# Performance work log

Measured on AMD Instinct MI355X. Metric: run time of the kernel, lower is better.

The kernel has to match this reference:

```python
import jax, jax.numpy as jnp
import numpy as np

B, S, D, H = 4, 2048, 1024, 16
DH = D // H
THETA = 10000.0
STD = (2.0 / (D + D)) ** 0.5


def _rope(x):
    # x: [..., S, DH]; positions are arange(S). Rotate interleaved pairs.
    half = DH // 2
    inv_freq = THETA ** (-jnp.arange(half, dtype=jnp.float32) * 2.0 / DH)  # [half]
    ang = jnp.arange(S, dtype=jnp.float32)[:, None] * inv_freq[None, :]   # [S, half]
    cos, sin = jnp.cos(ang), jnp.sin(ang)
    x1, x2 = x[..., 0::2], x[..., 1::2]
    o1 = x1 * cos - x2 * sin
    o2 = x1 * sin + x2 * cos
    return jnp.stack([o1, o2], axis=-1).reshape(x.shape)


def setup_inputs() -> dict:
    key = jax.random.key(0)
    kx, kq, kk, kv, ko = jax.random.split(key, 5)
    return {
        "x": jax.random.normal(kx, (B, S, D), dtype=jnp.float32),
        "wq": jax.random.normal(kq, (D, D), dtype=jnp.float32) * STD,
        "wk": jax.random.normal(kk, (D, D), dtype=jnp.float32) * STD,
        "wv": jax.random.normal(kv, (D, D), dtype=jnp.float32) * STD,
        "wo": jax.random.normal(ko, (D, D), dtype=jnp.float32) * STD,
    }


def reference(x, wq, wk, wv, wo):
    # fused QKV projection (Linear with no bias: x @ W.T)
    wqkv = jnp.concatenate([wq, wk, wv], axis=0)          # [3D, D]
    qkv = jnp.einsum('bsd,ed->bse', x, wqkv)              # [B, S, 3D]
    q, k, v = jnp.split(qkv, 3, axis=-1)
    # [B, H, S, DH]
    q = q.reshape(B, S, H, DH).transpose(0, 2, 1, 3)
    k = k.reshape(B, S, H, DH).transpose(0, 2, 1, 3)
    v = v.reshape(B, S, H, DH).transpose(0, 2, 1, 3)
    q = _rope(q)
    k = _rope(k)
    scale = 1.0 / jnp.sqrt(jnp.asarray(DH, dtype=q.dtype))
    scores = jnp.einsum('bhqd,bhkd->bhqk', q, k) * scale  # [B, H, S, S]
    causal = jnp.tril(jnp.ones((S, S), dtype=bool))
    scores = jnp.where(causal, scores, -jnp.inf)
    attn = jax.nn.softmax(scores, axis=-1)
    out = jnp.einsum('bhqk,bhkd->bhqd', attn, v)          # [B, H, S, DH]
    out = out.transpose(0, 2, 1, 3).reshape(B, S, D)
    return jnp.einsum('bsd,ed->bse', out, wo)             # output proj
```

## Files before the change

kernel.cpp:

```cpp
#include <hip/hip_runtime.h>
#include <cmath>


#define S_LEN 2048
#define NHEAD 16
#define DHEAD 64

typedef short bf16x8 __attribute__((ext_vector_type(8)));
typedef float f32x4  __attribute__((ext_vector_type(4)));

__device__ __forceinline__ float bf2f(unsigned short u) {
    unsigned x = ((unsigned)u) << 16;
    return __builtin_bit_cast(float, x);
}
__device__ __forceinline__ unsigned short f2bf(float f) {
    unsigned u = __builtin_bit_cast(unsigned, f);
    unsigned r = u + 0x7fff + ((u >> 16) & 1);
    return (unsigned short)(r >> 16);
}
__device__ __forceinline__ unsigned pack2(float lo, float hi) {
    return (unsigned)f2bf(lo) | ((unsigned)f2bf(hi) << 16);
}
__device__ __forceinline__ void gl16(const void* g, void* l) {
    __builtin_amdgcn_global_load_lds(
        (const __attribute__((address_space(1))) unsigned int*)g,
        (__attribute__((address_space(3))) unsigned int*)l, 16, 0, 0);
}

__global__ void cast_f32_bf16(const float* __restrict__ in,
                              unsigned* __restrict__ out, int n)
{
    const int i = (blockIdx.x * 256 + threadIdx.x) * 8;
    if (i >= n) return;
    const float4 a = *(const float4*)(in + i);
    const float4 b = *(const float4*)(in + i + 4);
    uint4 o;
    o.x = pack2(a.x, a.y); o.y = pack2(a.z, a.w);
    o.z = pack2(b.x, b.y); o.w = pack2(b.z, b.w);
    *(uint4*)(out + i / 2) = o;
}

__global__ void cast_w4(const float* __restrict__ wq, const float* __restrict__ wk,
                        const float* __restrict__ wv, const float* __restrict__ wo,
                        unsigned* __restrict__ Wb, unsigned* __restrict__ Wob)
{
    const int idx = blockIdx.x * 256 + threadIdx.x;
    const int sel = idx >> 17;
    const int loc = idx & 131071;
    const float* src = (sel == 0) ? wq : (sel == 1) ? wk : (sel == 2) ? wv : wo;
    unsigned* dst = (sel == 3) ? Wob : Wb + (size_t)sel * 524288;
    const int i = loc * 8;
    const float4 a = *(const float4*)(src + i);
    const float4 b = *(const float4*)(src + i + 4);
    uint4 o;
    o.x = pack2(a.x, a.y); o.y = pack2(a.z, a.w);
    o.z = pack2(b.x, b.y); o.w = pack2(b.z, b.w);
    *(uint4*)(dst + i / 2) = o;
}

template <int MODE>
__global__ __launch_bounds__(256, 2) void gemm_bt(
    const unsigned short* __restrict__ A,
    const unsigned short* __restrict__ Bw,
    unsigned short* __restrict__ Qb,
    unsigned short* __restrict__ Kb,
    unsigned short* __restrict__ Vt,
    float* __restrict__ Co)
{
    __shared__ __align__(16) unsigned short As[128 * 32];
    __shared__ __align__(16) unsigned short Bs[128 * 32];

    const int t    = threadIdx.x;
    const int bm   = blockIdx.x * 128;
    const int bn   = blockIdx.y * 128;
    const int lane = t & 63, wv = t >> 6;
    const int wr   = wv >> 1, wc = wv & 1;
    const int ln   = lane & 15, ko = lane >> 4;

    f32x4 acc[4][4];
    #pragma unroll
    for (int i = 0; i < 4; ++i)
        #pragma unroll
        for (int j = 0; j < 4; ++j)
            acc[i][j] = f32x4{0.f, 0.f, 0.f, 0.f};

    const int ar  = t >> 2;
    const int asg = t & 3;
    const unsigned short* aptr = A  + (size_t)(bm + ar) * 1024 + asg * 8;
    const unsigned short* bptr = Bw + (size_t)(bn + ar) * 1024 + asg * 8;

    for (int k0 = 0; k0 < 1024; k0 += 32) {
        __syncthreads();
        gl16(aptr + k0,               (char*)As + t * 16);
        gl16(aptr + k0 + 64 * 1024,   (char*)As + (t + 256) * 16);
        gl16(bptr + k0,               (char*)Bs + t * 16);
        gl16(bptr + k0 + 64 * 1024,   (char*)Bs + (t + 256) * 16);
        __syncthreads();

        bf16x8 af[4], bfr[4];
        #pragma unroll
        for (int i = 0; i < 4; ++i)
            af[i] = *(const bf16x8*)((const char*)As + (wr * 64 + i * 16 + ln) * 64 + ko * 16);
        #pragma unroll
        for (int j = 0; j < 4; ++j)
            bfr[j] = *(const bf16x8*)((const char*)Bs + (wc * 64 + j * 16 + ln) * 64 + ko * 16);
        #pragma unroll
        for (int i = 0; i < 4; ++i)
            #pragma unroll
            for (int j = 0; j < 4; ++j)
                acc[i][j] = __builtin_amdgcn_mfma_f32_16x16x32_bf16(af[i], bfr[j], acc[i][j], 0, 0, 0);
    }

    #pragma unroll
    for (int i = 0; i < 4; ++i) {
        const int mb = bm + wr * 64 + i * 16 + ko * 4;
        #pragma unroll
        for (int j = 0; j < 4; ++j) {
            const int n = bn + wc * 64 + j * 16 + ln;
            if constexpr (MODE == 0) {
                const int which = n >> 10, nh = n & 1023;
                const int h = nh >> 6, dh = nh & 63;
                const int bb = mb >> 11, s = mb & 2047;
                const int bh = bb * NHEAD + h;
                if (which == 2) {
                    uint2 pk;
                    pk.x = pack2(acc[i][j][0], acc[i][j][1]);
                    pk.y = pack2(acc[i][j][2], acc[i][j][3]);
                    *(uint2*)&Vt[((size_t)bh * 64 + dh) * 2048 + s] = pk;
                } else {
                    unsigned short* dst = which ? Kb : Qb;
                    #pragma unroll
                    for (int r = 0; r < 4; ++r)
                        dst[((size_t)bh * 2048 + (s + r)) * 64 + dh] = f2bf(acc[i][j][r]);
                }
            } else {
                #pragma unroll
                for (int r = 0; r < 4; ++r)
                    Co[(size_t)(mb + r) * 1024 + n] = acc[i][j][r];
            }
        }
    }
}

__global__ void rope_kernel(unsigned int* __restrict__ Qb, unsigned int* __restrict__ Kb)
{
    const int idx  = blockIdx.x * 256 + threadIdx.x;
    const int i    = idx & 31;
    const int srow = (idx >> 5) & 2047;

    const float inv = powf(10000.0f, -(float)i * (1.0f / 32.0f));
    const float ang = (float)srow * inv;
    float sn, cs;
    sincosf(ang, &sn, &cs);

    const unsigned q = Qb[idx];
    const unsigned k = Kb[idx];
    const float qx = bf2f((unsigned short)(q & 0xffff)), qy = bf2f((unsigned short)(q >> 16));
    const float kx = bf2f((unsigned short)(k & 0xffff)), ky = bf2f((unsigned short)(k >> 16));
    Qb[idx] = pack2(qx * cs - qy * sn, qx * sn + qy * cs);
    Kb[idx] = pack2(kx * cs - ky * sn, kx * sn + ky * cs);
}

__device__ __forceinline__ void process_tile(
    const char* __restrict__ Ks, const char* __restrict__ Vs, char* pb,
    const bf16x8 qf[2], f32x4 ao[4], float& m_i, float& l_i,
    int ln, int koct, int qrow, bool diag)
{
    f32x4 sv[4];
    #pragma unroll
    for (int nf = 0; nf < 4; ++nf) sv[nf] = f32x4{0.f, 0.f, 0.f, 0.f};
    #pragma unroll
    for (int s = 0; s < 2; ++s) {
        #pragma unroll
        for (int nf = 0; nf < 4; ++nf) {
            const int key = nf * 16 + ln;
            const bf16x8 kf = *(const bf16x8*)(Ks + key * 128 + (((s * 4 + koct) ^ (key & 7)) * 16));
            sv[nf] = __builtin_amdgcn_mfma_f32_16x16x32_bf16(kf, qf[s], sv[nf], 0, 0, 0);
        }
    }

    if (diag) {
        #pragma unroll
        for (int nf = 0; nf < 4; ++nf) {
            #pragma unroll
            for (int r = 0; r < 4; ++r)
                if (nf * 16 + koct * 4 + r > qrow) sv[nf][r] = -INFINITY;
        }
    }

    float mx = sv[0][0];
    #pragma unroll
    for (int nf = 0; nf < 4; ++nf)
        #pragma unroll
        for (int r = 0; r < 4; ++r) mx = fmaxf(mx, sv[nf][r]);
    mx = fmaxf(mx, __shfl_xor(mx, 16));
    mx = fmaxf(mx, __shfl_xor(mx, 32));
    const float mn = fmaxf(m_i, mx);
    const float al = __expf(m_i - mn);
    m_i = mn;
    float sum = 0.f;
    #pragma unroll
    for (int nf = 0; nf < 4; ++nf)
        #pragma unroll
        for (int r = 0; r < 4; ++r) {
            const float pv = __expf(sv[nf][r] - mn);
            sv[nf][r] = pv;
            sum += pv;
        }
    sum += __shfl_xor(sum, 16);
    sum += __shfl_xor(sum, 32);
    l_i = l_i * al + sum;

    float alr[4];
    #pragma unroll
    for (int r = 0; r < 4; ++r) alr[r] = __shfl(al, koct * 4 + r);
    #pragma unroll
    for (int nf = 0; nf < 4; ++nf)
        #pragma unroll
        for (int r = 0; r < 4; ++r)
            ao[nf][r] *= alr[r];

    #pragma unroll
    for (int nf = 0; nf < 4; ++nf) {
        uint2 pk;
        pk.x = pack2(sv[nf][0], sv[nf][1]);
        pk.y = pack2(sv[nf][2], sv[nf][3]);
        *(uint2*)(pb + ln * 128 + ((nf * 32 + koct * 8) ^ ((ln & 7) << 4))) = pk;
    }

    #pragma unroll
    for (int s2 = 0; s2 < 2; ++s2) {
        const bf16x8 pa = *(const bf16x8*)(pb + ln * 128 + (((s2 * 4 + koct) ^ (ln & 7)) * 16));
        #pragma unroll
        for (int nf = 0; nf < 4; ++nf) {
            const int dh = nf * 16 + ln;
            const bf16x8 vf = *(const bf16x8*)(Vs + dh * 128 + (((s2 * 4 + koct) ^ (dh & 7)) * 16));
            ao[nf] = __builtin_amdgcn_mfma_f32_16x16x32_bf16(pa, vf, ao[nf], 0, 0, 0);
        }
    }
}

__global__ __launch_bounds__(256, 3) void attn_mfma(
    const unsigned short* __restrict__ Qb,
    const unsigned short* __restrict__ Kb,
    const unsigned short* __restrict__ Vt,
    unsigned short* __restrict__ Aot)
{
    __shared__ __align__(16) unsigned short Ksh[2][64 * 64];
    __shared__ __align__(16) unsigned short Vsh[2][64 * 64];
    __shared__ __align__(16) unsigned short Psh[4 * 16 * 64];

    const int t    = threadIdx.x;
    const int lane = t & 63, w = t >> 6;
    const int ln   = lane & 15, koct = lane >> 4;
    const int bid  = blockIdx.x;
    const int qtA  = (bid >> 3) & 15;
    const int qtB  = 31 - qtA;
    const int bh   = (bid & 7) + 8 * (bid >> 7);
    const int rA   = qtA * 64, rB = qtB * 64;
    const size_t kvbase = (size_t)bh * S_LEN * DHEAD;
    const size_t vtbase = (size_t)bh * DHEAD * S_LEN;

    bf16x8 qfA[2], qfB[2];
    #pragma unroll
    for (int s = 0; s < 2; ++s) {
        bf16x8 va = *(const bf16x8*)(Qb + kvbase + (size_t)(rA + w * 16 + ln) * 64 + s * 32 + koct * 8);
        bf16x8 vb = *(const bf16x8*)(Qb + kvbase + (size_t)(rB + w * 16 + ln) * 64 + s * 32 + koct * 8);
        #pragma unroll
        for (int j = 0; j < 8; ++j) {
            va[j] = (short)f2bf(bf2f((unsigned short)va[j]) * 0.125f);
            vb[j] = (short)f2bf(bf2f((unsigned short)vb[j]) * 0.125f);
        }
        qfA[s] = va; qfB[s] = vb;
    }

    f32x4 aoA[4], aoB[4];
    float mA = -INFINITY, lA = 0.f, mB = -INFINITY, lB = 0.f;
    #pragma unroll
    for (int nf = 0; nf < 4; ++nf) { aoA[nf] = f32x4{0.f,0.f,0.f,0.f}; aoB[nf] = f32x4{0.f,0.f,0.f,0.f}; }

    const int kr = t >> 3;
    const int sg = t & 7;
    const int kr2 = kr + 32;
    const int qrow = w * 16 + ln;

    gl16(Kb + kvbase + (size_t)kr  * 64 + (sg ^ (kr  & 7)) * 8, (char*)&Ksh[0][0] + t * 16);
    gl16(Kb + kvbase + (size_t)kr2 * 64 + (sg ^ (kr2 & 7)) * 8, (char*)&Ksh[0][0] + (t + 256) * 16);
    gl16(Vt + vtbase + (size_t)kr  * S_LEN + (sg ^ (kr  & 7)) * 8, (char*)&Vsh[0][0] + t * 16);
    gl16(Vt + vtbase + (size_t)kr2 * S_LEN + (sg ^ (kr2 & 7)) * 8, (char*)&Vsh[0][0] + (t + 256) * 16);
    __syncthreads();

    char* pb = (char*)Psh + w * 2048;
    int cur = 0;

    for (int kt = 0; kt <= qtB; ++kt) {
        if (kt < qtB) {
            const int c1 = (kt + 1) * 64;
            gl16(Kb + kvbase + (size_t)(c1 + kr)  * 64 + (sg ^ (kr  & 7)) * 8, (char*)&Ksh[cur ^ 1][0] + t * 16);
            gl16(Kb + kvbase + (size_t)(c1 + kr2) * 64 + (sg ^ (kr2 & 7)) * 8, (char*)&Ksh[cur ^ 1][0] + (t + 256) * 16);
            gl16(Vt + vtbase + (size_t)kr  * S_LEN + c1 + (sg ^ (kr  & 7)) * 8, (char*)&Vsh[cur ^ 1][0] + t * 16);
            gl16(Vt + vtbase + (size_t)kr2 * S_LEN + c1 + (sg ^ (kr2 & 7)) * 8, (char*)&Vsh[cur ^ 1][0] + (t + 256) * 16);
        }

        const char* Ks = (const char*)&Ksh[cur][0];
        const char* Vs = (const char*)&Vsh[cur][0];

        process_tile(Ks, Vs, pb, qfB, aoB, mB, lB, ln, koct, qrow, kt == qtB);
        if (kt <= qtA)
            process_tile(Ks, Vs, pb, qfA, aoA, mA, lA, ln, koct, qrow, kt == qtA);

        __syncthreads();
        cur ^= 1;
    }

    const int b = bh >> 4, h = bh & 15;
    float lAr[4], lBr[4];
    #pragma unroll
    for (int r = 0; r < 4; ++r) {
        lAr[r] = __shfl(lA, koct * 4 + r);
        lBr[r] = __shfl(lB, koct * 4 + r);
    }
    #pragma unroll
    for (int r = 0; r < 4; ++r) {
        const float invA = 1.0f / lAr[r];
        const float invB = 1.0f / lBr[r];
        const int sA = rA + w * 16 + koct * 4 + r;
        const int sB = rB + w * 16 + koct * 4 + r;
        #pragma unroll
        for (int nf = 0; nf < 4; ++nf) {
            Aot[(size_t)(b * S_LEN + sA) * 1024 + h * 64 + nf * 16 + ln] = f2bf(aoA[nf][r] * invA);
            Aot[(size_t)(b * S_LEN + sB) * 1024 + h * 64 + nf * 16 + ln] = f2bf(aoB[nf][r] * invB);
        }
    }
}

extern "C" void kernel_launch(void* const* d_in, const int* in_sizes, int n_in,
                              void* d_out, int out_size, void* d_ws, size_t ws_size,
                              hipStream_t stream)
{
    const float* x  = (const float*)d_in[0];
    const float* wq = (const float*)d_in[1];
    const float* wk = (const float*)d_in[2];
    const float* wv = (const float*)d_in[3];
    const float* wo = (const float*)d_in[4];
    float* out = (float*)d_out;

    char* p = (char*)d_ws;
    unsigned short* Xb  = (unsigned short*)p;
    unsigned short* Wb  = (unsigned short*)(p + ((size_t)16 << 20));
    unsigned short* Wob = (unsigned short*)(p + ((size_t)22 << 20));
    unsigned short* Qb  = (unsigned short*)(p + ((size_t)24 << 20));
    unsigned short* Kb  = (unsigned short*)(p + ((size_t)40 << 20));
    unsigned short* Vt  = (unsigned short*)(p + ((size_t)56 << 20));
    unsigned short* Aot = (unsigned short*)(p + ((size_t)72 << 20));

    const int NX = 8192 * 1024;
    cast_f32_bf16<<<NX / 2048, 256, 0, stream>>>(x, (unsigned*)Xb, NX);
    cast_w4<<<2048, 256, 0, stream>>>(wq, wk, wv, wo, (unsigned*)Wb, (unsigned*)Wob);

    gemm_bt<0><<<dim3(64, 24), 256, 0, stream>>>(Xb, Wb, Qb, Kb, Vt, nullptr);
    rope_kernel<<<16384, 256, 0, stream>>>((unsigned int*)Qb, (unsigned int*)Kb);
    attn_mfma<<<1024, 256, 0, stream>>>(Qb, Kb, Vt, Aot);
    gemm_bt<1><<<dim3(64, 8), 256, 0, stream>>>(Aot, Wob, nullptr, nullptr, nullptr, out);
}
```

Before: 293.3 us.

## Double-buffer GEMM LDS tiles and add lazy softmax rescaling in attention

The projection GEMM now keeps two LDS buffers per operand and issues the next k-slice's global-to-LDS loads before computing the current slice, halving barriers per k-step and overlapping load latency with MFMA work. The launch-bounds occupancy hint rises from 2 to 3 blocks per CU, even though LDS use per block doubles. In the flash-attention inner loop, the running-max update and accumulator rescale are skipped unless some lane's new max exceeds the old by more than 8 (FA4-style lazy rescaling). This saves exp and multiply work at the cost of exponentials up to e^8 before normalization, which fp32 tolerates.

```diff
diff --git a/kernel.cpp b/kernel.cpp
--- a/kernel.cpp
+++ b/kernel.cpp
@@ -59,7 +59,7 @@
 }
 
 template <int MODE>
-__global__ __launch_bounds__(256, 2) void gemm_bt(
+__global__ __launch_bounds__(256, 3) void gemm_bt(
     const unsigned short* __restrict__ A,
     const unsigned short* __restrict__ Bw,
     unsigned short* __restrict__ Qb,
@@ -67,8 +67,8 @@
     unsigned short* __restrict__ Vt,
     float* __restrict__ Co)
 {
-    __shared__ __align__(16) unsigned short As[128 * 32];
-    __shared__ __align__(16) unsigned short Bs[128 * 32];
+    __shared__ __align__(16) unsigned short As[2][128 * 32];
+    __shared__ __align__(16) unsigned short Bs[2][128 * 32];
 
     const int t    = threadIdx.x;
     const int bm   = blockIdx.x * 128;
@@ -89,27 +89,46 @@
     const unsigned short* aptr = A  + (size_t)(bm + ar) * 1024 + asg * 8;
     const unsigned short* bptr = Bw + (size_t)(bn + ar) * 1024 + asg * 8;
 
-    for (int k0 = 0; k0 < 1024; k0 += 32) {
+    #define STAGE(k0, buf)                                                          \
+        do {                                                                        \
+            gl16(aptr + (k0),             (char*)&As[buf][0] + t * 16);             \
+            gl16(aptr + (k0) + 64 * 1024, (char*)&As[buf][0] + (t + 256) * 16);     \
+            gl16(bptr + (k0),             (char*)&Bs[buf][0] + t * 16);             \
+            gl16(bptr + (k0) + 64 * 1024, (char*)&Bs[buf][0] + (t + 256) * 16);     \
+        } while (0)
+
+    #define COMPUTE(buf)                                                            \
+        do {                                                                        \
+            bf16x8 af[4], bfr[4];                                                   \
+            _Pragma("unroll")                                                       \
+            for (int i = 0; i < 4; ++i)                                             \
+                af[i] = *(const bf16x8*)((const char*)&As[buf][0] +                 \
+                         (wr * 64 + i * 16 + ln) * 64 + ko * 16);                   \
+            _Pragma("unroll")                                                       \
+            for (int j = 0; j < 4; ++j)                                             \
+                bfr[j] = *(const bf16x8*)((const char*)&Bs[buf][0] +                \
+                         (wc * 64 + j * 16 + ln) * 64 + ko * 16);                   \
+            _Pragma("unroll")                                                       \
+            for (int i = 0; i < 4; ++i)                                             \
+                _Pragma("unroll")                                                   \
+                for (int j = 0; j < 4; ++j)                                         \
+                    acc[i][j] = __builtin_amdgcn_mfma_f32_16x16x32_bf16(            \
+                        af[i], bfr[j], acc[i][j], 0, 0, 0);                         \
+        } while (0)
+
+    STAGE(0, 0);
+    __syncthreads();
+
+    for (int k0 = 0; k0 < 1024; k0 += 64) {
+        if (k0 + 32 < 1024) STAGE(k0 + 32, 1);
+        COMPUTE(0);
         __syncthreads();
-        gl16(aptr + k0,               (char*)As + t * 16);
-        gl16(aptr + k0 + 64 * 1024,   (char*)As + (t + 256) * 16);
-        gl16(bptr + k0,               (char*)Bs + t * 16);
-        gl16(bptr + k0 + 64 * 1024,   (char*)Bs + (t + 256) * 16);
+        if (k0 + 64 < 1024) STAGE(k0 + 64, 0);
+        COMPUTE(1);
         __syncthreads();
-
-        bf16x8 af[4], bfr[4];
-        #pragma unroll
-        for (int i = 0; i < 4; ++i)
-            af[i] = *(const bf16x8*)((const char*)As + (wr * 64 + i * 16 + ln) * 64 + ko * 16);
-        #pragma unroll
-        for (int j = 0; j < 4; ++j)
-            bfr[j] = *(const bf16x8*)((const char*)Bs + (wc * 64 + j * 16 + ln) * 64 + ko * 16);
-        #pragma unroll
-        for (int i = 0; i < 4; ++i)
-            #pragma unroll
-            for (int j = 0; j < 4; ++j)
-                acc[i][j] = __builtin_amdgcn_mfma_f32_16x16x32_bf16(af[i], bfr[j], acc[i][j], 0, 0, 0);
-    }
+    }
+    #undef STAGE
+    #undef COMPUTE
 
     #pragma unroll
     for (int i = 0; i < 4; ++i) {
@@ -195,30 +214,34 @@
         for (int r = 0; r < 4; ++r) mx = fmaxf(mx, sv[nf][r]);
     mx = fmaxf(mx, __shfl_xor(mx, 16));
     mx = fmaxf(mx, __shfl_xor(mx, 32));
-    const float mn = fmaxf(m_i, mx);
-    const float al = __expf(m_i - mn);
-    m_i = mn;
+
+    if (!__all(mx <= m_i + 8.0f)) {
+        const float mn = fmaxf(m_i, mx);
+        const float al = __expf(m_i - mn);
+        m_i = mn;
+        l_i *= al;
+        float alr[4];
+        #pragma unroll
+        for (int r = 0; r < 4; ++r) alr[r] = __shfl(al, koct * 4 + r);
+        #pragma unroll
+        for (int nf = 0; nf < 4; ++nf)
+            #pragma unroll
+            for (int r = 0; r < 4; ++r)
+                ao[nf][r] *= alr[r];
+    }
+
     float sum = 0.f;
     #pragma unroll
     for (int nf = 0; nf < 4; ++nf)
         #pragma unroll
         for (int r = 0; r < 4; ++r) {
-            const float pv = __expf(sv[nf][r] - mn);
+            const float pv = __expf(sv[nf][r] - m_i);
             sv[nf][r] = pv;
             sum += pv;
         }
     sum += __shfl_xor(sum, 16);
     sum += __shfl_xor(sum, 32);
-    l_i = l_i * al + sum;
-
-    float alr[4];
-    #pragma unroll
-    for (int r = 0; r < 4; ++r) alr[r] = __shfl(al, koct * 4 + r);
-    #pragma unroll
-    for (int nf = 0; nf < 4; ++nf)
-        #pragma unroll
-        for (int r = 0; r < 4; ++r)
-            ao[nf][r] *= alr[r];
+    l_i += sum;
 
     #pragma unroll
     for (int nf = 0; nf < 4; ++nf) {
```

New measurement: 293.1 us. Within noise of the previous version (-0.1%).
